# Kernel tuning notes

Measured on AMD Instinct MI355X. Metric: run time of the kernel, lower is better.

The kernel has to match this reference:

```python
import jax, jax.numpy as jnp
import numpy as np

B, T, C = 2, 2048, 1024
E, K = 8, 2            # n_experts, top_k (n_experts_active)
H = 2736               # round8(int(4*C*2/3)) SwiGLU hidden dim


def setup_inputs() -> dict:
    key = jax.random.key(0)
    ks = jax.random.split(key, 8)
    def w(k, shape, fan_in):
        return jax.random.normal(k, shape, jnp.float32) * (1.0 / np.sqrt(fan_in))
    x = jax.random.normal(ks[0], (B, T, C), jnp.float32)
    router_w = w(ks[1], (C, E), C)          # gate.weight.T
    wg = w(ks[2], (E, C, H), C)             # stacked expert w_gate.weight.T
    wu = w(ks[3], (E, C, H), C)             # stacked expert w_up.weight.T
    wd = w(ks[4], (E, H, C), H)             # stacked expert w_down.weight.T
    sg = w(ks[5], (C, H), C)                # shared expert gate
    su = w(ks[6], (C, H), C)                # shared expert up
    sd = w(ks[7], (H, C), H)                # shared expert down
    return {"x": x, "router_w": router_w, "wg": wg, "wu": wu, "wd": wd,
            "sg": sg, "su": su, "sd": sd}


def reference(x, router_w, wg, wu, wd, sg, su, sd):
    Bx, Tx, Cx = x.shape
    xf = x.reshape(-1, Cx)                       # (Tk, C)
    Tk = xf.shape[0]

    # --- router ---
    logits = xf @ router_w                       # (Tk, E)
    top_v, top_i = jax.lax.top_k(logits, K)      # (Tk, K)
    rw = jax.nn.softmax(top_v, axis=-1)          # normalized weights over selected

    # combine weights per (token, expert): scatter router weights
    rows = jnp.arange(Tk)[:, None]
    w_te = jnp.zeros((Tk, E), xf.dtype).at[rows, top_i].add(rw)   # (Tk, E)

    # --- experts (dense dispatch; weight w_te zeros out unselected experts) ---
    gate = jnp.einsum('tc,ech->teh', xf, wg)     # (Tk, E, H)
    up = jnp.einsum('tc,ech->teh', xf, wu)
    h = jax.nn.silu(gate) * up                   # SwiGLU hidden
    out = jnp.einsum('teh,te,ehc->tc', h, w_te, wd)   # weighted combine

    # --- shared expert ---
    out = out + (jax.nn.silu(xf @ sg) * (xf @ su)) @ sd

    # --- aux load-balancing loss ---
    mask = jnp.zeros((Tk, E), xf.dtype).at[rows, top_i].add(1.0)
    f = mask.mean(axis=0) / K
    p = jax.nn.softmax(logits, axis=-1).mean(axis=0)
    aux_loss = E * (f * p).sum()

    return out.reshape(Bx, Tx, Cx), aux_loss
```

## Files before the change

### kernel.cpp

```cpp
#include <hip/hip_runtime.h>

typedef _Float16 f16;
typedef _Float16 f16x4 __attribute__((ext_vector_type(4)));
typedef _Float16 f16x8 __attribute__((ext_vector_type(8)));
typedef float f32x4 __attribute__((ext_vector_type(4)));

#define TK 4096
#define CD 1024
#define HD 2736
#define HP 2816
#define MT 104
#define RC 13312

#define GLDS16(ldsp, gp) __builtin_amdgcn_global_load_lds( \
    (const __attribute__((address_space(1))) unsigned int*)(gp), \
    (__attribute__((address_space(3))) unsigned int*)(ldsp), 16, 0, 0)

static constexpr size_t WS_XB  = 0;
static constexpr size_t WS_H   = WS_XB  + (size_t)TK*CD*2;
static constexpr size_t WS_WGT = WS_H   + (size_t)RC*HP*2;
static constexpr size_t WS_WUT = WS_WGT + (size_t)8*HP*CD*2;
static constexpr size_t WS_WDT = WS_WUT + (size_t)8*HP*CD*2;
static constexpr size_t WS_SGT = WS_WDT + (size_t)8*CD*HP*2;
static constexpr size_t WS_SUT = WS_SGT + (size_t)HP*CD*2;
static constexpr size_t WS_SDT = WS_SUT + (size_t)HP*CD*2;
static constexpr size_t WS_CT  = WS_SDT + (size_t)CD*HP*2;
static constexpr size_t WS_OBUF = WS_WGT;
static constexpr size_t CT_STOK = 0;
static constexpr size_t CT_SW   = CT_STOK + (size_t)RC*4;
static constexpr size_t CT_TI   = CT_SW   + (size_t)RC*4;
static constexpr size_t CT_TW   = CT_TI   + (size_t)TK*2*4;
static constexpr size_t CT_ISL  = CT_TW   + (size_t)TK*2*4;
static constexpr size_t CT_CNT  = CT_ISL  + (size_t)TK*2*4;
static constexpr size_t CT_PS   = CT_CNT  + 32;
static constexpr size_t CT_CUR  = CT_PS   + 32;
static constexpr size_t CT_OFF  = CT_CUR  + 32;
static constexpr size_t CT_SIZE = CT_OFF  + 64;

__global__ __launch_bounds__(256) void k_tr(
    const float* __restrict__ srcMain, f16* __restrict__ dstMain,
    const float* __restrict__ srcSh,   f16* __restrict__ dstSh,
    int R, int Cc, int Rp, int Cp, int nMain,
    size_t sstride, size_t dstride) {
    const float* src; f16* dst;
    if ((int)blockIdx.z < nMain) {
        src = srcMain + (size_t)blockIdx.z * sstride;
        dst = dstMain + (size_t)blockIdx.z * dstride;
    } else {
        src = srcSh; dst = dstSh;
    }
    const int tid = threadIdx.x;
    const int l = tid & 63, w = tid >> 6;
    const int cc0 = blockIdx.x * 128 + w * 32 + (l >> 3) * 4;
    const int rr0 = blockIdx.y * 64 + (l & 7) * 8;
    float4 v[8];
    #pragma unroll
    for (int e = 0; e < 8; e++) {
        int gr = rr0 + e;
        if (gr < R && cc0 + 3 < Cc) {
            v[e] = *(const float4*)(src + (size_t)gr * Cc + cc0);
        } else {
            float* ve = (float*)&v[e];
            #pragma unroll
            for (int c = 0; c < 4; c++)
                ve[c] = (gr < R && cc0 + c < Cc) ? src[(size_t)gr * Cc + cc0 + c] : 0.f;
        }
    }
    #pragma unroll
    for (int c = 0; c < 4; c++) {
        const float* vp = (const float*)v;
        f16x8 o = { (f16)vp[0*4+c], (f16)vp[1*4+c], (f16)vp[2*4+c], (f16)vp[3*4+c],
                    (f16)vp[4*4+c], (f16)vp[5*4+c], (f16)vp[6*4+c], (f16)vp[7*4+c] };
        *(f16x8*)(dst + (size_t)(cc0 + c) * Rp + rr0) = o;
    }
}

__global__ void k_router(const float* __restrict__ x, const float* __restrict__ rw,
                         f16* __restrict__ xb,
                         int* __restrict__ topi, float* __restrict__ topw,
                         int* __restrict__ cnt, float* __restrict__ psum) {
    __shared__ float pl[8];
    int tid = threadIdx.x;
    if (tid < 8) pl[tid] = 0.f;
    __syncthreads();
    int wave = tid >> 6, lane = tid & 63;
    int t = blockIdx.x * 4 + wave;
    float acc[8];
    #pragma unroll
    for (int e = 0; e < 8; e++) acc[e] = 0.f;
    const float* xr = x + (size_t)t * CD;
    f16* xbr = xb + (size_t)t * CD;
    for (int i = 0; i < CD / 64; i++) {
        int c = lane + i * 64;
        float xv = xr[c];
        xbr[c] = (f16)xv;
        const float* wr = rw + c * 8;
        #pragma unroll
        for (int e = 0; e < 8; e++) acc[e] = fmaf(xv, wr[e], acc[e]);
    }
    #pragma unroll
    for (int e = 0; e < 8; e++) {
        #pragma unroll
        for (int off = 32; off; off >>= 1) acc[e] += __shfl_xor(acc[e], off);
    }
    if (lane == 0) {
        float v1 = -1e30f; int i1 = 0;
        #pragma unroll
        for (int e = 0; e < 8; e++) if (acc[e] > v1) { v1 = acc[e]; i1 = e; }
        float v2 = -1e30f; int i2 = (i1 == 0) ? 1 : 0;
        #pragma unroll
        for (int e = 0; e < 8; e++) if (e != i1 && acc[e] > v2) { v2 = acc[e]; i2 = e; }
        float b = expf(v2 - v1);
        float w1 = 1.f / (1.f + b);
        topi[t*2] = i1; topi[t*2+1] = i2;
        topw[t*2] = w1; topw[t*2+1] = b * w1;
        atomicAdd(&cnt[i1], 1);
        atomicAdd(&cnt[i2], 1);
        float m = acc[0];
        #pragma unroll
        for (int e = 1; e < 8; e++) m = fmaxf(m, acc[e]);
        float pe[8]; float s = 0.f;
        #pragma unroll
        for (int e = 0; e < 8; e++) { pe[e] = expf(acc[e] - m); s += pe[e]; }
        float inv = 1.f / s;
        #pragma unroll
        for (int e = 0; e < 8; e++) atomicAdd(&pl[e], pe[e] * inv);
    }
    __syncthreads();
    if (tid < 8) atomicAdd(&psum[tid], pl[tid]);
}

__global__ void k_prefix(const int* __restrict__ cnt, int* __restrict__ cur,
                         int* __restrict__ offs) {
    if (threadIdx.x == 0 && blockIdx.x == 0) {
        int off = 0;
        for (int e = 0; e < 8; e++) {
            offs[e] = off; cur[e] = off;
            off += (cnt[e] + 127) & ~127;
        }
        offs[8] = off;
        offs[9] = RC;
    }
}

__global__ void k_scatter(const int* __restrict__ topi, const float* __restrict__ topw,
                          int* __restrict__ cur, const int* __restrict__ offs,
                          int* __restrict__ stok, float* __restrict__ sw,
                          int* __restrict__ islot) {
    int t = blockIdx.x * 256 + threadIdx.x;
    if (t >= TK) return;
    #pragma unroll
    for (int s = 0; s < 2; s++) {
        int e = topi[t*2 + s];
        int pos = atomicAdd(&cur[e], 1);
        stok[pos] = t;
        sw[pos] = topw[t*2 + s];
        islot[t*2 + s] = pos;
    }
    int base = offs[8];
    stok[base + t] = t;
    sw[base + t] = 1.0f;
}

__global__ __launch_bounds__(256, 2) void k_ffn1(
    const f16* __restrict__ xb, const f16* __restrict__ wgt,
    const f16* __restrict__ wut, const f16* __restrict__ sgt,
    const f16* __restrict__ sut, const int* __restrict__ offs,
    const int* __restrict__ cnt, const int* __restrict__ stok,
    f16* __restrict__ hbuf)
{
    __shared__ f16 As[128*32];
    __shared__ f16 Bg[128*32];
    __shared__ f16 Bu[128*32];

    const int n0 = blockIdx.x * 128;
    const int m0 = blockIdx.y * 128;
    int g = 0;
    while (g < 8 && m0 >= offs[g+1]) g++;
    if (m0 >= offs[8] + TK) return;
    if (g < 8 && (m0 - offs[g]) >= cnt[g]) return;

    const f16* __restrict__ Wg = (g < 8) ? wgt + (size_t)g * HP * CD : sgt;
    const f16* __restrict__ Wu = (g < 8) ? wut + (size_t)g * HP * CD : sut;

    const int tid = threadIdx.x;
    const int lane = tid & 63;
    const int w = tid >> 6;
    const int r0  = w * 32 + (lane >> 2);
    const int kof = (lane & 3) * 8;
    const f16* pa0 = xb + (size_t)stok[m0 + r0]      * CD + kof;
    const f16* pa1 = xb + (size_t)stok[m0 + r0 + 16] * CD + kof;
    const f16* pg0 = Wg + (size_t)(n0 + r0)      * CD + kof;
    const f16* pg1 = Wg + (size_t)(n0 + r0 + 16) * CD + kof;
    const f16* pu0 = Wu + (size_t)(n0 + r0)      * CD + kof;
    const f16* pu1 = Wu + (size_t)(n0 + r0 + 16) * CD + kof;
    f16* const lA = As + w * 1024;
    f16* const lG = Bg + w * 1024;
    f16* const lU = Bu + w * 1024;

    f32x4 accg[4][4], accu[4][4];
    #pragma unroll
    for (int i = 0; i < 4; i++)
        #pragma unroll
        for (int j = 0; j < 4; j++)
            #pragma unroll
            for (int r = 0; r < 4; r++) { accg[i][j][r] = 0.f; accu[i][j][r] = 0.f; }

    const int wm = (w >> 1) * 64;
    const int wn = (w & 1) * 64;
    const int fm = lane & 15;
    const int fq = lane >> 4;

    for (int k0 = 0; k0 < CD; k0 += 32) {
        GLDS16(lA,       pa0 + k0);
        GLDS16(lA + 512, pa1 + k0);
        GLDS16(lG,       pg0 + k0);
        GLDS16(lG + 512, pg1 + k0);
        GLDS16(lU,       pu0 + k0);
        GLDS16(lU + 512, pu1 + k0);
        __syncthreads();
        f16x8 af[4];
        #pragma unroll
        for (int mi = 0; mi < 4; mi++)
            af[mi] = *(const f16x8*)&As[(wm + mi*16 + fm) * 32 + fq * 8];
        #pragma unroll
        for (int ni = 0; ni < 4; ni++) {
            f16x8 bgf = *(const f16x8*)&Bg[(wn + ni*16 + fm) * 32 + fq * 8];
            f16x8 buf = *(const f16x8*)&Bu[(wn + ni*16 + fm) * 32 + fq * 8];
            #pragma unroll
            for (int mi = 0; mi < 4; mi++) {
                accg[mi][ni] = __builtin_amdgcn_mfma_f32_16x16x32_f16(af[mi], bgf, accg[mi][ni], 0, 0, 0);
                accu[mi][ni] = __builtin_amdgcn_mfma_f32_16x16x32_f16(af[mi], buf, accu[mi][ni], 0, 0, 0);
            }
        }
        __syncthreads();
    }

    #pragma unroll
    for (int mi = 0; mi < 4; mi++) {
        #pragma unroll
        for (int ni = 0; ni < 4; ni++) {
            #pragma unroll
            for (int r = 0; r < 4; r++) {
                int row = m0 + wm + mi*16 + fq*4 + r;
                int col = n0 + wn + ni*16 + fm;
                float gv = accg[mi][ni][r];
                float uv = accu[mi][ni][r];
                float hv = gv / (1.f + __expf(-gv)) * uv;
                hbuf[(size_t)row * HP + col] = (f16)hv;
            }
        }
    }
}

__global__ __launch_bounds__(256, 2) void k_ffn2(
    const f16* __restrict__ hbuf, const f16* __restrict__ wdt,
    const f16* __restrict__ sdt, const int* __restrict__ offs,
    const int* __restrict__ cnt, float* __restrict__ obuf)
{
    __shared__ f16 As[128*32];
    __shared__ f16 Bs[128*32];

    const int n0 = blockIdx.x * 128;
    const int m0 = blockIdx.y * 128;
    int g = 0;
    while (g < 8 && m0 >= offs[g+1]) g++;
    if (m0 >= offs[8] + TK) return;
    if (g < 8 && (m0 - offs[g]) >= cnt[g]) return;
    const f16* __restrict__ W = (g < 8) ? wdt + (size_t)g * CD * HP : sdt;

    const int tid = threadIdx.x;
    const int lane = tid & 63;
    const int w = tid >> 6;
    const int r0  = w * 32 + (lane >> 2);
    const int kof = (lane & 3) * 8;
    const f16* pa0 = hbuf + (size_t)(m0 + r0)      * HP + kof;
    const f16* pa1 = hbuf + (size_t)(m0 + r0 + 16) * HP + kof;
    const f16* pb0 = W + (size_t)(n0 + r0)      * HP + kof;
    const f16* pb1 = W + (size_t)(n0 + r0 + 16) * HP + kof;
    f16* const lA = As + w * 1024;
    f16* const lB = Bs + w * 1024;

    f32x4 acc[4][4];
    #pragma unroll
    for (int i = 0; i < 4; i++)
        #pragma unroll
        for (int j = 0; j < 4; j++)
            #pragma unroll
            for (int r = 0; r < 4; r++) acc[i][j][r] = 0.f;

    const int wm = (w >> 1) * 64;
    const int wn = (w & 1) * 64;
    const int fm = lane & 15;
    const int fq = lane >> 4;

    for (int k0 = 0; k0 < HP; k0 += 32) {
        GLDS16(lA,       pa0 + k0);
        GLDS16(lA + 512, pa1 + k0);
        GLDS16(lB,       pb0 + k0);
        GLDS16(lB + 512, pb1 + k0);
        __syncthreads();
        f16x8 af[4];
        #pragma unroll
        for (int mi = 0; mi < 4; mi++)
            af[mi] = *(const f16x8*)&As[(wm + mi*16 + fm) * 32 + fq * 8];
        #pragma unroll
        for (int ni = 0; ni < 4; ni++) {
            f16x8 bfr = *(const f16x8*)&Bs[(wn + ni*16 + fm) * 32 + fq * 8];
            #pragma unroll
            for (int mi = 0; mi < 4; mi++)
                acc[mi][ni] = __builtin_amdgcn_mfma_f32_16x16x32_f16(af[mi], bfr, acc[mi][ni], 0, 0, 0);
        }
        __syncthreads();
    }

    #pragma unroll
    for (int mi = 0; mi < 4; mi++) {
        #pragma unroll
        for (int r = 0; r < 4; r++) {
            int row = m0 + wm + mi*16 + fq*4 + r;
            #pragma unroll
            for (int ni = 0; ni < 4; ni++) {
                int col = n0 + wn + ni*16 + fm;
                obuf[(size_t)row * CD + col] = acc[mi][ni][r];
            }
        }
    }
}

__global__ __launch_bounds__(256) void k_comb(
    const float* __restrict__ obuf, const int* __restrict__ islot,
    const float* __restrict__ topw, const int* __restrict__ offs,
    float* __restrict__ out)
{
    const int t = blockIdx.x;
    const int c = threadIdx.x * 4;
    const int s0 = islot[t*2], s1 = islot[t*2+1];
    const float w0 = topw[t*2], w1 = topw[t*2+1];
    const int sh = offs[8] + t;
    float4 a = *(const float4*)(obuf + (size_t)s0 * CD + c);
    float4 b = *(const float4*)(obuf + (size_t)s1 * CD + c);
    float4 s = *(const float4*)(obuf + (size_t)sh * CD + c);
    float4 o;
    o.x = fmaf(w0, a.x, fmaf(w1, b.x, s.x));
    o.y = fmaf(w0, a.y, fmaf(w1, b.y, s.y));
    o.z = fmaf(w0, a.z, fmaf(w1, b.z, s.z));
    o.w = fmaf(w0, a.w, fmaf(w1, b.w, s.w));
    *(float4*)(out + (size_t)t * CD + c) = o;
}

__global__ void k_aux(const int* __restrict__ cnt, const float* __restrict__ psum,
                      float* __restrict__ out_aux) {
    if (threadIdx.x == 0 && blockIdx.x == 0) {
        float a = 0.f;
        for (int e = 0; e < 8; e++) {
            float f = (float)cnt[e] / ((float)TK * 2.f);
            float p = psum[e] / (float)TK;
            a += f * p;
        }
        out_aux[0] = 8.f * a;
    }
}

extern "C" void kernel_launch(void* const* d_in, const int* in_sizes, int n_in,
                              void* d_out, int out_size, void* d_ws, size_t ws_size,
                              hipStream_t stream) {
    const float* x  = (const float*)d_in[0];
    const float* rw = (const float*)d_in[1];
    const float* wg = (const float*)d_in[2];
    const float* wu = (const float*)d_in[3];
    const float* wd = (const float*)d_in[4];
    const float* sg = (const float*)d_in[5];
    const float* su = (const float*)d_in[6];
    const float* sd = (const float*)d_in[7];
    float* out = (float*)d_out;

    char* ws = (char*)d_ws;
    f16* xb   = (f16*)(ws + WS_XB);
    f16* hbuf = (f16*)(ws + WS_H);
    f16* wgt  = (f16*)(ws + WS_WGT);
    f16* wut  = (f16*)(ws + WS_WUT);
    f16* wdt  = (f16*)(ws + WS_WDT);
    f16* sgt  = (f16*)(ws + WS_SGT);
    f16* sut  = (f16*)(ws + WS_SUT);
    f16* sdt  = (f16*)(ws + WS_SDT);
    float* obuf = (float*)(ws + WS_OBUF);
    char* ct  = ws + WS_CT;
    int*   stok = (int*)  (ct + CT_STOK);
    float* swt  = (float*)(ct + CT_SW);
    int*   topi = (int*)  (ct + CT_TI);
    float* topw = (float*)(ct + CT_TW);
    int*   isl  = (int*)  (ct + CT_ISL);
    int*   cnt  = (int*)  (ct + CT_CNT);
    float* psum = (float*)(ct + CT_PS);
    int*   cur  = (int*)  (ct + CT_CUR);
    int*   offs = (int*)  (ct + CT_OFF);

    hipMemsetAsync(ct, 0, CT_SIZE, stream);

    k_router<<<dim3(TK / 4), dim3(256), 0, stream>>>(x, rw, xb, topi, topw, cnt, psum);
    k_prefix<<<dim3(1), dim3(64), 0, stream>>>(cnt, cur, offs);
    k_scatter<<<dim3(TK / 256), dim3(256), 0, stream>>>(topi, topw, cur, offs, stok, swt, isl);

    k_tr<<<dim3(HP/128, CD/64, 9), dim3(256), 0, stream>>>(
        wg, wgt, sg, sgt, CD, HD, CD, HP, 8, (size_t)CD*HD, (size_t)HP*CD);
    k_tr<<<dim3(HP/128, CD/64, 9), dim3(256), 0, stream>>>(
        wu, wut, su, sut, CD, HD, CD, HP, 8, (size_t)CD*HD, (size_t)HP*CD);
    k_tr<<<dim3(CD/128, HP/64, 9), dim3(256), 0, stream>>>(
        wd, wdt, sd, sdt, HD, CD, HP, CD, 8, (size_t)HD*CD, (size_t)CD*HP);

    k_ffn1<<<dim3(HP/128, MT), dim3(256), 0, stream>>>(xb, wgt, wut, sgt, sut, offs, cnt, stok, hbuf);
    k_ffn2<<<dim3(CD/128, MT), dim3(256), 0, stream>>>(hbuf, wdt, sdt, offs, cnt, obuf);
    k_comb<<<dim3(TK), dim3(256), 0, stream>>>(obuf, isl, topw, offs, out);
    k_aux<<<dim3(1), dim3(64), 0, stream>>>(cnt, psum, out + (size_t)TK * CD);
}
```

Before: 800.3 us.

## Double K tile to 64 with XOR-swizzled LDS layout in both FFN GEMMs

Both grouped FFN GEMM kernels now stage a 64-wide K slice per iteration instead of 32. This halves the number of barrier pairs per K loop. Global-to-LDS loads are reorganised so each wave loads 8 rows of 64 halves, with the 16-byte chunk index XOR-swizzled by row; fragment reads apply the matching swizzle to avoid LDS bank conflicts. LDS use doubles, to 48KB in ffn1 and 32KB in ffn2, which may pressure occupancy at two blocks per CU. Offsets are now 32-bit int, which could overflow for large buffers.

```diff
diff --git a/kernel.cpp b/kernel.cpp
--- a/kernel.cpp
+++ b/kernel.cpp
@@ -169,9 +169,9 @@
     const int* __restrict__ cnt, const int* __restrict__ stok,
     f16* __restrict__ hbuf)
 {
-    __shared__ f16 As[128*32];
-    __shared__ f16 Bg[128*32];
-    __shared__ f16 Bu[128*32];
+    __shared__ f16 As[128*64];
+    __shared__ f16 Bg[128*64];
+    __shared__ f16 Bu[128*64];
 
     const int n0 = blockIdx.x * 128;
     const int m0 = blockIdx.y * 128;
@@ -186,17 +186,14 @@
     const int tid = threadIdx.x;
     const int lane = tid & 63;
     const int w = tid >> 6;
-    const int r0  = w * 32 + (lane >> 2);
-    const int kof = (lane & 3) * 8;
-    const f16* pa0 = xb + (size_t)stok[m0 + r0]      * CD + kof;
-    const f16* pa1 = xb + (size_t)stok[m0 + r0 + 16] * CD + kof;
-    const f16* pg0 = Wg + (size_t)(n0 + r0)      * CD + kof;
-    const f16* pg1 = Wg + (size_t)(n0 + r0 + 16) * CD + kof;
-    const f16* pu0 = Wu + (size_t)(n0 + r0)      * CD + kof;
-    const f16* pu1 = Wu + (size_t)(n0 + r0 + 16) * CD + kof;
-    f16* const lA = As + w * 1024;
-    f16* const lG = Bg + w * 1024;
-    f16* const lU = Bu + w * 1024;
+    const int w32 = w * 32;
+
+    const int asw = (((lane & 7) ^ (lane >> 3)) << 3);
+    int rA[4];
+    #pragma unroll
+    for (int i = 0; i < 4; i++)
+        rA[i] = stok[m0 + w32 + 8*i + (lane >> 3)] * CD + asw;
+    const int rB = (n0 + w32 + (lane >> 3)) * CD + asw;
 
     f32x4 accg[4][4], accu[4][4];
     #pragma unroll
@@ -210,27 +207,32 @@
     const int wn = (w & 1) * 64;
     const int fm = lane & 15;
     const int fq = lane >> 4;
-
-    for (int k0 = 0; k0 < CD; k0 += 32) {
-        GLDS16(lA,       pa0 + k0);
-        GLDS16(lA + 512, pa1 + k0);
-        GLDS16(lG,       pg0 + k0);
-        GLDS16(lG + 512, pg1 + k0);
-        GLDS16(lU,       pu0 + k0);
-        GLDS16(lU + 512, pu1 + k0);
+    const int fs = fm & 7;
+
+    for (int k0 = 0; k0 < CD; k0 += 64) {
+        #pragma unroll
+        for (int i = 0; i < 4; i++) {
+            GLDS16(&As[(w32 + 8*i) * 64], xb + rA[i] + k0);
+            GLDS16(&Bg[(w32 + 8*i) * 64], Wg + rB + i*8*CD + k0);
+            GLDS16(&Bu[(w32 + 8*i) * 64], Wu + rB + i*8*CD + k0);
+        }
         __syncthreads();
-        f16x8 af[4];
-        #pragma unroll
-        for (int mi = 0; mi < 4; mi++)
-            af[mi] = *(const f16x8*)&As[(wm + mi*16 + fm) * 32 + fq * 8];
-        #pragma unroll
-        for (int ni = 0; ni < 4; ni++) {
-            f16x8 bgf = *(const f16x8*)&Bg[(wn + ni*16 + fm) * 32 + fq * 8];
-            f16x8 buf = *(const f16x8*)&Bu[(wn + ni*16 + fm) * 32 + fq * 8];
-            #pragma unroll
-            for (int mi = 0; mi < 4; mi++) {
-                accg[mi][ni] = __builtin_amdgcn_mfma_f32_16x16x32_f16(af[mi], bgf, accg[mi][ni], 0, 0, 0);
-                accu[mi][ni] = __builtin_amdgcn_mfma_f32_16x16x32_f16(af[mi], buf, accu[mi][ni], 0, 0, 0);
+        #pragma unroll
+        for (int kk = 0; kk < 2; kk++) {
+            const int sw = ((((kk << 2) | fq) ^ fs) << 3);
+            f16x8 af[4];
+            #pragma unroll
+            for (int mi = 0; mi < 4; mi++)
+                af[mi] = *(const f16x8*)&As[(wm + mi*16 + fm) * 64 + sw];
+            #pragma unroll
+            for (int ni = 0; ni < 4; ni++) {
+                f16x8 bgf = *(const f16x8*)&Bg[(wn + ni*16 + fm) * 64 + sw];
+                f16x8 bur = *(const f16x8*)&Bu[(wn + ni*16 + fm) * 64 + sw];
+                #pragma unroll
+                for (int mi = 0; mi < 4; mi++) {
+                    accg[mi][ni] = __builtin_amdgcn_mfma_f32_16x16x32_f16(af[mi], bgf, accg[mi][ni], 0, 0, 0);
+                    accu[mi][ni] = __builtin_amdgcn_mfma_f32_16x16x32_f16(af[mi], bur, accu[mi][ni], 0, 0, 0);
+                }
             }
         }
         __syncthreads();
@@ -258,8 +260,8 @@
     const f16* __restrict__ sdt, const int* __restrict__ offs,
     const int* __restrict__ cnt, float* __restrict__ obuf)
 {
-    __shared__ f16 As[128*32];
-    __shared__ f16 Bs[128*32];
+    __shared__ f16 As[128*64];
+    __shared__ f16 Bs[128*64];
 
     const int n0 = blockIdx.x * 128;
     const int m0 = blockIdx.y * 128;
@@ -272,14 +274,11 @@
     const int tid = threadIdx.x;
     const int lane = tid & 63;
     const int w = tid >> 6;
-    const int r0  = w * 32 + (lane >> 2);
-    const int kof = (lane & 3) * 8;
-    const f16* pa0 = hbuf + (size_t)(m0 + r0)      * HP + kof;
-    const f16* pa1 = hbuf + (size_t)(m0 + r0 + 16) * HP + kof;
-    const f16* pb0 = W + (size_t)(n0 + r0)      * HP + kof;
-    const f16* pb1 = W + (size_t)(n0 + r0 + 16) * HP + kof;
-    f16* const lA = As + w * 1024;
-    f16* const lB = Bs + w * 1024;
+    const int w32 = w * 32;
+
+    const int asw = (((lane & 7) ^ (lane >> 3)) << 3);
+    const int rA = (m0 + w32 + (lane >> 3)) * HP + asw;
+    const int rB = (n0 + w32 + (lane >> 3)) * HP + asw;
 
     f32x4 acc[4][4];
     #pragma unroll
@@ -293,23 +292,29 @@
     const int wn = (w & 1) * 64;
     const int fm = lane & 15;
     const int fq = lane >> 4;
-
-    for (int k0 = 0; k0 < HP; k0 += 32) {
-        GLDS16(lA,       pa0 + k0);
-        GLDS16(lA + 512, pa1 + k0);
-        GLDS16(lB,       pb0 + k0);
-        GLDS16(lB + 512, pb1 + k0);
+    const int fs = fm & 7;
+
+    for (int k0 = 0; k0 < HP; k0 += 64) {
+        #pragma unroll
+        for (int i = 0; i < 4; i++) {
+            GLDS16(&As[(w32 + 8*i) * 64], hbuf + (size_t)rA + i*8*HP + k0);
+            GLDS16(&Bs[(w32 + 8*i) * 64], W    + (size_t)rB + i*8*HP + k0);
+        }
         __syncthreads();
-        f16x8 af[4];
-        #pragma unroll
-        for (int mi = 0; mi < 4; mi++)
-            af[mi] = *(const f16x8*)&As[(wm + mi*16 + fm) * 32 + fq * 8];
-        #pragma unroll
-        for (int ni = 0; ni < 4; ni++) {
-            f16x8 bfr = *(const f16x8*)&Bs[(wn + ni*16 + fm) * 32 + fq * 8];
+        #pragma unroll
+        for (int kk = 0; kk < 2; kk++) {
+            const int sw = ((((kk << 2) | fq) ^ fs) << 3);
+            f16x8 af[4];
             #pragma unroll
             for (int mi = 0; mi < 4; mi++)
-                acc[mi][ni] = __builtin_amdgcn_mfma_f32_16x16x32_f16(af[mi], bfr, acc[mi][ni], 0, 0, 0);
+                af[mi] = *(const f16x8*)&As[(wm + mi*16 + fm) * 64 + sw];
+            #pragma unroll
+            for (int ni = 0; ni < 4; ni++) {
+                f16x8 bfr = *(const f16x8*)&Bs[(wn + ni*16 + fm) * 64 + sw];
+                #pragma unroll
+                for (int mi = 0; mi < 4; mi++)
+                    acc[mi][ni] = __builtin_amdgcn_mfma_f32_16x16x32_f16(af[mi], bfr, acc[mi][ni], 0, 0, 0);
+            }
         }
         __syncthreads();
     }
```

New measurement: 774.2 us. 1.03x faster.
